# Kernel tuning notes

Hardware: AMD Instinct MI355X
Metric: run time of the kernel (lower is better)

The kernel has to match this reference:

```python
import jax, jax.numpy as jnp
import numpy as np


def setup_inputs() -> dict:
    key = jax.random.key(0)
    k1, k2 = jax.random.split(key)
    x = jax.random.normal(k1, (4096, 1024), dtype=jnp.float32)  # [B, D] queries
    y = jax.random.normal(k2, (8192, 1024), dtype=jnp.float32)  # [N, D] database
    return {"x": x, "y": y}


def reference(x, y):
    # -sum((x[:, None, :] - y[None, :, :])**2, -1)  computed via the
    x_sq = jnp.sum(x * x, axis=-1)              # [B]
    y_sq = jnp.sum(y * y, axis=-1)              # [N]
    xy = jnp.einsum('bd,nd->bn', x, y)          # [B, N]
    return -(x_sq[:, None] - 2.0 * xy + y_sq[None, :])  # [B, N]
```

## Files before the change

### kernel.cpp

```cpp
#include <hip/hip_runtime.h>
#include <hip/hip_bf16.h>


typedef __attribute__((ext_vector_type(4))) int i32x4;

#define BM 256
#define BN 256
#define KD 1024
#define NT 8

__device__ __forceinline__ void gld16(const void* g, void* l) {
    __builtin_amdgcn_global_load_lds(
        (const __attribute__((address_space(1))) unsigned int*)g,
        (__attribute__((address_space(3))) unsigned int*)l,
        16, 0, 0);
}

#define BAR()   asm volatile("s_barrier" ::: "memory")
#define LGKM0() asm volatile("s_waitcnt lgkmcnt(0)" ::: "memory")

__global__ __launch_bounds__(256) void prep_q(
    const float* __restrict__ x, const float* __restrict__ y,
    signed char* __restrict__ xq, signed char* __restrict__ yq,
    float* __restrict__ sx, float* __restrict__ sy,
    float* __restrict__ xsq, float* __restrict__ ysq, int M, int N)
{
    int row = blockIdx.x;
    const float* src;
    signed char* dst;
    float* nrm;
    float* scl;
    float sfac;
    if (row < M) {
        src = x + (size_t)row * KD; dst = xq + (size_t)row * KD;
        nrm = xsq + row; scl = sx + row; sfac = 2.0f;
    } else {
        int r = row - M;
        src = y + (size_t)r * KD; dst = yq + (size_t)r * KD;
        nrm = ysq + r; scl = sy + r; sfac = 1.0f;
    }
    int t = threadIdx.x;
    float4 v = ((const float4*)src)[t];
    float ss = v.x * v.x + v.y * v.y + v.z * v.z + v.w * v.w;
    float am = fmaxf(fmaxf(fabsf(v.x), fabsf(v.y)),
                     fmaxf(fabsf(v.z), fabsf(v.w)));
    #pragma unroll
    for (int off = 32; off > 0; off >>= 1) {
        ss += __shfl_down(ss, off, 64);
        am = fmaxf(am, __shfl_down(am, off, 64));
    }
    __shared__ float rs[4], rm[4];
    if ((t & 63) == 0) { rs[t >> 6] = ss; rm[t >> 6] = am; }
    __syncthreads();
    float tots = rs[0] + rs[1] + rs[2] + rs[3];
    float totm = fmaxf(fmaxf(rm[0], rm[1]), fmaxf(rm[2], rm[3]));
    float inv = totm > 0.0f ? 127.0f / totm : 0.0f;

    int q0 = (int)rintf(v.x * inv), q1 = (int)rintf(v.y * inv);
    int q2 = (int)rintf(v.z * inv), q3 = (int)rintf(v.w * inv);
    q0 = max(-127, min(127, q0)); q1 = max(-127, min(127, q1));
    q2 = max(-127, min(127, q2)); q3 = max(-127, min(127, q3));
    int packed = (q0 & 255) | ((q1 & 255) << 8) |
                 ((q2 & 255) << 16) | ((q3 & 255) << 24);
    ((int*)dst)[t] = packed;
    if (t == 0) { *nrm = tots; *scl = sfac * totm / 127.0f; }
}

__global__ __launch_bounds__(512, 2) void gemm_i8(
    const signed char* __restrict__ xq, const signed char* __restrict__ yq,
    const float* __restrict__ sx, const float* __restrict__ sy,
    const float* __restrict__ xsq, const float* __restrict__ ysq,
    float* __restrict__ out, int M, int N)
{
    __shared__ __align__(16) char lds[131072];

    const int ntm = M / BM;
    const int ntn = N / BN;
    const int bid = blockIdx.x;
    int tm, tn;
    if (ntm == 16 && ntn == 32) {
        int xcd = bid & 7, k = bid >> 3;
        tm = (xcd >> 2) * 8 + (k >> 3);
        tn = (xcd & 3) * 8 + (k & 7);
    } else {
        tm = bid / ntn;
        tn = bid % ntn;
    }

    const int tid  = threadIdx.x;
    const int wid  = tid >> 6;
    const int lane = tid & 63;
    const int wm   = wid >> 2;
    const int wn   = wid & 3;
    const int l15  = lane & 15;
    const int hi   = lane >> 4;
    const int s8   = lane & 7;

    const int r8  = lane >> 3;
    const int cbs = s8 ^ (r8 & 7);
    const signed char* aBase = xq + (size_t)(tm * BM + wid * 16 + r8) * KD + cbs * 16;
    const signed char* bBase = yq + (size_t)(tn * BN + wid * 16 + r8) * KD + cbs * 16;
    const int dstBase = wid * 2048 + lane * 16;

    #define STAGE_A(kt, h) do {                                               \
        const signed char* g_ = aBase + (size_t)(h) * 128 * KD + (size_t)(kt) * 128; \
        char* d_ = &lds[((kt) & 1) * 32768 + (h) * 16384 + dstBase];          \
        gld16(g_, d_); gld16(g_ + 8 * KD, d_ + 1024);                         \
    } while (0)
    #define STAGE_B(kt, h) do {                                               \
        const signed char* g_ = bBase + (size_t)(h) * 128 * KD + (size_t)(kt) * 128; \
        char* d_ = &lds[65536 + ((kt) & 1) * 32768 + (h) * 16384 + dstBase];  \
        gld16(g_, d_); gld16(g_ + 8 * KD, d_ + 1024);                         \
    } while (0)

    int aro[4], bro[2], xk[2];
    #pragma unroll
    for (int i = 0; i < 4; ++i) aro[i] = (wm * 64 + i * 16 + l15) * 128;
    #pragma unroll
    for (int j = 0; j < 2; ++j) bro[j] = (wn * 32 + j * 16 + l15) * 128;
    xk[0] = ((0 + hi) ^ s8) * 16;
    xk[1] = ((4 + hi) ^ s8) * 16;

    i32x4 acc[2][4][2][2] = {};
    i32x4 aF[2][4];
    i32x4 bF[2][2][2];

    #define MFMA_Q(mq, nq) do {                                              \
        _Pragma("unroll") for (int ks = 0; ks < 2; ++ks)                     \
        _Pragma("unroll") for (int i = 0; i < 4; ++i)                        \
        _Pragma("unroll") for (int j = 0; j < 2; ++j)                        \
            acc[mq][i][nq][j] = __builtin_amdgcn_mfma_i32_16x16x64_i8(       \
                aF[ks][i], bF[nq][ks][j], acc[mq][i][nq][j], 0, 0, 0);       \
    } while (0)

    STAGE_A(0, 0); STAGE_B(0, 0);
    STAGE_A(0, 1); STAGE_B(0, 1);
    STAGE_A(1, 0); STAGE_B(1, 0);
    asm volatile("s_waitcnt vmcnt(8)" ::: "memory");
    BAR();

    for (int s = 0; s < NT; ++s) {
        const int ab = (s & 1) * 32768;
        const int bb = 65536 + ab;

        #pragma unroll
        for (int ks = 0; ks < 2; ++ks) {
            #pragma unroll
            for (int i = 0; i < 4; ++i)
                aF[ks][i] = *(const i32x4*)&lds[ab + aro[i] + xk[ks]];
            #pragma unroll
            for (int j = 0; j < 2; ++j)
                bF[0][ks][j] = *(const i32x4*)&lds[bb + bro[j] + xk[ks]];
        }
        if (s + 1 < NT) STAGE_A(s + 1, 1);
        asm volatile("s_waitcnt lgkmcnt(8)" ::: "memory");
        BAR();
        LGKM0();
        __builtin_amdgcn_sched_barrier(0);
        __builtin_amdgcn_s_setprio(1);
        MFMA_Q(0, 0);
        __builtin_amdgcn_s_setprio(0);
        if (s < NT - 1) {
            asm volatile("s_waitcnt vmcnt(6)" ::: "memory");
        } else {
            asm volatile("s_waitcnt vmcnt(0)" ::: "memory");
        }
        BAR();

        #pragma unroll
        for (int ks = 0; ks < 2; ++ks)
            #pragma unroll
            for (int j = 0; j < 2; ++j)
                bF[1][ks][j] = *(const i32x4*)&lds[bb + 16384 + bro[j] + xk[ks]];
        if (s + 1 < NT) STAGE_B(s + 1, 1);
        BAR();
        LGKM0();
        __builtin_amdgcn_sched_barrier(0);
        __builtin_amdgcn_s_setprio(1);
        MFMA_Q(0, 1);
        __builtin_amdgcn_s_setprio(0);
        BAR();

        #pragma unroll
        for (int ks = 0; ks < 2; ++ks)
            #pragma unroll
            for (int i = 0; i < 4; ++i)
                aF[ks][i] = *(const i32x4*)&lds[ab + 16384 + aro[i] + xk[ks]];
        if (s + 2 < NT) STAGE_A(s + 2, 0);
        BAR();
        LGKM0();
        __builtin_amdgcn_sched_barrier(0);
        __builtin_amdgcn_s_setprio(1);
        MFMA_Q(1, 0);
        __builtin_amdgcn_s_setprio(0);
        BAR();

        if (s + 2 < NT) STAGE_B(s + 2, 0);
        __builtin_amdgcn_s_setprio(1);
        MFMA_Q(1, 1);
        __builtin_amdgcn_s_setprio(0);
        if (s < NT - 2) {
            asm volatile("s_waitcnt vmcnt(8)" ::: "memory");
        } else if (s == NT - 2) {
            asm volatile("s_waitcnt vmcnt(4)" ::: "memory");
        }
        BAR();
    }

    #pragma unroll
    for (int mq = 0; mq < 2; ++mq)
        #pragma unroll
        for (int i = 0; i < 4; ++i) {
            int r0 = tm * BM + mq * 128 + wm * 64 + i * 16 + hi * 4;
            #pragma unroll
            for (int nq = 0; nq < 2; ++nq)
                #pragma unroll
                for (int j = 0; j < 2; ++j) {
                    int c = tn * BN + nq * 128 + wn * 32 + j * 16 + l15;
                    float syv = sy[c];
                    float ysv = ysq[c];
                    #pragma unroll
                    for (int r = 0; r < 4; ++r) {
                        int row = r0 + r;
                        out[(size_t)row * N + c] =
                            sx[row] * syv * (float)acc[mq][i][nq][j][r]
                            - xsq[row] - ysv;
                    }
                }
        }
}

__global__ __launch_bounds__(256) void fallback_l2(
    const float* __restrict__ x, const float* __restrict__ y,
    float* __restrict__ out, int M, int N, int K)
{
    int tx = threadIdx.x & 15, ty = threadIdx.x >> 4;
    int row = blockIdx.y * 16 + ty;
    int col = blockIdx.x * 16 + tx;
    __shared__ float xs[16][17], ys[16][17];
    float s = 0.f;
    for (int k0 = 0; k0 < K; k0 += 16) {
        xs[ty][tx] = x[(size_t)row * K + k0 + tx];
        ys[ty][tx] = y[(size_t)(blockIdx.x * 16 + ty) * K + k0 + tx];
        __syncthreads();
        #pragma unroll
        for (int kk = 0; kk < 16; ++kk) {
            float d = xs[ty][kk] - ys[tx][kk];
            s += d * d;
        }
        __syncthreads();
    }
    out[(size_t)row * N + col] = -s;
}

extern "C" void kernel_launch(void* const* d_in, const int* in_sizes, int n_in,
                              void* d_out, int out_size, void* d_ws, size_t ws_size,
                              hipStream_t stream) {
    const float* x = (const float*)d_in[0];
    const float* y = (const float*)d_in[1];
    float* out = (float*)d_out;
    const int M = in_sizes[0] / KD;
    const int N = in_sizes[1] / KD;

    size_t need = (size_t)(M + N) * KD
                + (size_t)(M + N) * 2 * sizeof(float) + 256;
    if (ws_size >= need && M == 4096 && N == 8192) {
        char* w = (char*)d_ws;
        signed char* xq = (signed char*)w;
        signed char* yq = xq + (size_t)M * KD;
        float* sx  = (float*)(yq + (size_t)N * KD);
        float* sy  = sx + M;
        float* xsq = sy + N;
        float* ysq = xsq + M;

        prep_q<<<M + N, 256, 0, stream>>>(x, y, xq, yq, sx, sy, xsq, ysq, M, N);
        int grid = (M / BM) * (N / BN);
        gemm_i8<<<grid, 512, 0, stream>>>(xq, yq, sx, sy, xsq, ysq, out, M, N);
    } else {
        dim3 g(N / 16, M / 16);
        fallback_l2<<<g, 256, 0, stream>>>(x, y, out, M, N, KD);
    }
}
```

Baseline: 66.43 us.

## Replace hand-scheduled 8-wave i8 GEMM with simple 16-wave double-buffered loop

The int8 GEMM moves from 512 threads (8 waves, each owning a 2x2 set of quadrant sub-tiles) to 1024 threads (16 waves in a 4x4 grid, each owning a 64x64 output sub-tile). The hand-interleaved quadrant pipeline with explicit vmcnt/lgkmcnt waits and raw s_barriers is replaced by a plain double-buffered loop that prefetches the next K-tile, then runs 32 MFMAs per step and ends each step with __syncthreads. The goal is simpler code and more waves to hide latency in place of manual scheduling. The cost is fewer accumulator registers per wave under the new launch bounds and less fine-grained overlap of loads with MFMAs. The new launch bounds (1024, 4) request more resident waves than the 128 KiB LDS tile per block likely allows, so that occupancy may not be reached.

```diff
diff --git a/kernel.cpp b/kernel.cpp
--- a/kernel.cpp
+++ b/kernel.cpp
@@ -15,9 +15,6 @@
         (__attribute__((address_space(3))) unsigned int*)l,
         16, 0, 0);
 }
-
-#define BAR()   asm volatile("s_barrier" ::: "memory")
-#define LGKM0() asm volatile("s_waitcnt lgkmcnt(0)" ::: "memory")
 
 __global__ __launch_bounds__(256) void prep_q(
     const float* __restrict__ x, const float* __restrict__ y,
@@ -66,7 +63,7 @@
     if (t == 0) { *nrm = tots; *scl = sfac * totm / 127.0f; }
 }
 
-__global__ __launch_bounds__(512, 2) void gemm_i8(
+__global__ __launch_bounds__(1024, 4) void gemm_i8(
     const signed char* __restrict__ xq, const signed char* __restrict__ yq,
     const float* __restrict__ sx, const float* __restrict__ sy,
     const float* __restrict__ xsq, const float* __restrict__ ysq,
@@ -90,144 +87,82 @@
     const int tid  = threadIdx.x;
     const int wid  = tid >> 6;
     const int lane = tid & 63;
-    const int wm   = wid >> 2;
-    const int wn   = wid & 3;
+    const int wr   = wid >> 2;
+    const int wc   = wid & 3;
     const int l15  = lane & 15;
     const int hi   = lane >> 4;
-    const int s8   = lane & 7;
-
-    const int r8  = lane >> 3;
-    const int cbs = s8 ^ (r8 & 7);
-    const signed char* aBase = xq + (size_t)(tm * BM + wid * 16 + r8) * KD + cbs * 16;
-    const signed char* bBase = yq + (size_t)(tn * BN + wid * 16 + r8) * KD + cbs * 16;
-    const int dstBase = wid * 2048 + lane * 16;
-
-    #define STAGE_A(kt, h) do {                                               \
-        const signed char* g_ = aBase + (size_t)(h) * 128 * KD + (size_t)(kt) * 128; \
-        char* d_ = &lds[((kt) & 1) * 32768 + (h) * 16384 + dstBase];          \
-        gld16(g_, d_); gld16(g_ + 8 * KD, d_ + 1024);                         \
+
+    const int r128 = tid >> 3;
+    const int cbs  = (tid & 7) ^ (r128 & 7);
+    const signed char* aBase = xq + (size_t)(tm * BM + r128) * KD + cbs * 16;
+    const signed char* bBase = yq + (size_t)(tn * BN + r128) * KD + cbs * 16;
+    const int dstB = tid * 16;
+
+    #define STAGE(kt, buf) do {                                               \
+        const signed char* ga_ = aBase + (size_t)(kt) * 128;                  \
+        const signed char* gb_ = bBase + (size_t)(kt) * 128;                  \
+        char* da_ = &lds[(buf) * 32768 + dstB];                               \
+        char* db_ = &lds[65536 + (buf) * 32768 + dstB];                       \
+        gld16(ga_, da_); gld16(ga_ + 128 * KD, da_ + 16384);                  \
+        gld16(gb_, db_); gld16(gb_ + 128 * KD, db_ + 16384);                  \
     } while (0)
-    #define STAGE_B(kt, h) do {                                               \
-        const signed char* g_ = bBase + (size_t)(h) * 128 * KD + (size_t)(kt) * 128; \
-        char* d_ = &lds[65536 + ((kt) & 1) * 32768 + (h) * 16384 + dstBase];  \
-        gld16(g_, d_); gld16(g_ + 8 * KD, d_ + 1024);                         \
-    } while (0)
-
-    int aro[4], bro[2], xk[2];
-    #pragma unroll
-    for (int i = 0; i < 4; ++i) aro[i] = (wm * 64 + i * 16 + l15) * 128;
-    #pragma unroll
-    for (int j = 0; j < 2; ++j) bro[j] = (wn * 32 + j * 16 + l15) * 128;
-    xk[0] = ((0 + hi) ^ s8) * 16;
-    xk[1] = ((4 + hi) ^ s8) * 16;
-
-    i32x4 acc[2][4][2][2] = {};
-    i32x4 aF[2][4];
-    i32x4 bF[2][2][2];
-
-    #define MFMA_Q(mq, nq) do {                                              \
-        _Pragma("unroll") for (int ks = 0; ks < 2; ++ks)                     \
-        _Pragma("unroll") for (int i = 0; i < 4; ++i)                        \
-        _Pragma("unroll") for (int j = 0; j < 2; ++j)                        \
-            acc[mq][i][nq][j] = __builtin_amdgcn_mfma_i32_16x16x64_i8(       \
-                aF[ks][i], bF[nq][ks][j], acc[mq][i][nq][j], 0, 0, 0);       \
-    } while (0)
-
-    STAGE_A(0, 0); STAGE_B(0, 0);
-    STAGE_A(0, 1); STAGE_B(0, 1);
-    STAGE_A(1, 0); STAGE_B(1, 0);
-    asm volatile("s_waitcnt vmcnt(8)" ::: "memory");
-    BAR();
-
-    for (int s = 0; s < NT; ++s) {
-        const int ab = (s & 1) * 32768;
-        const int bb = 65536 + ab;
+
+    int aro[4], bro[4], xk[2];
+    #pragma unroll
+    for (int mi = 0; mi < 4; ++mi) aro[mi] = (wr * 64 + mi * 16 + l15) * 128;
+    #pragma unroll
+    for (int nj = 0; nj < 4; ++nj) bro[nj] = (wc * 64 + nj * 16 + l15) * 128;
+    xk[0] = ((0 + hi) ^ (l15 & 7)) * 16;
+    xk[1] = ((4 + hi) ^ (l15 & 7)) * 16;
+
+    i32x4 acc[4][4] = {};
+
+    STAGE(0, 0);
+    __syncthreads();
+
+    int buf = 0;
+    for (int t = 0; t < NT; ++t) {
+        if (t + 1 < NT) STAGE(t + 1, buf ^ 1);
+        const int ab = buf * 32768;
 
         #pragma unroll
         for (int ks = 0; ks < 2; ++ks) {
-            #pragma unroll
-            for (int i = 0; i < 4; ++i)
-                aF[ks][i] = *(const i32x4*)&lds[ab + aro[i] + xk[ks]];
-            #pragma unroll
-            for (int j = 0; j < 2; ++j)
-                bF[0][ks][j] = *(const i32x4*)&lds[bb + bro[j] + xk[ks]];
+            i32x4 aF[4], bF[4];
+            #pragma unroll
+            for (int mi = 0; mi < 4; ++mi)
+                aF[mi] = *(const i32x4*)&lds[ab + aro[mi] + xk[ks]];
+            #pragma unroll
+            for (int nj = 0; nj < 4; ++nj)
+                bF[nj] = *(const i32x4*)&lds[65536 + ab + bro[nj] + xk[ks]];
+            __builtin_amdgcn_s_setprio(1);
+            #pragma unroll
+            for (int mi = 0; mi < 4; ++mi)
+                #pragma unroll
+                for (int nj = 0; nj < 4; ++nj)
+                    acc[mi][nj] = __builtin_amdgcn_mfma_i32_16x16x64_i8(
+                        aF[mi], bF[nj], acc[mi][nj], 0, 0, 0);
+            __builtin_amdgcn_s_setprio(0);
         }
-        if (s + 1 < NT) STAGE_A(s + 1, 1);
-        asm volatile("s_waitcnt lgkmcnt(8)" ::: "memory");
-        BAR();
-        LGKM0();
-        __builtin_amdgcn_sched_barrier(0);
-        __builtin_amdgcn_s_setprio(1);
-        MFMA_Q(0, 0);
-        __builtin_amdgcn_s_setprio(0);
-        if (s < NT - 1) {
-            asm volatile("s_waitcnt vmcnt(6)" ::: "memory");
-        } else {
-            asm volatile("s_waitcnt vmcnt(0)" ::: "memory");
+        __syncthreads();
+        buf ^= 1;
+    }
+
+    #pragma unroll
+    for (int mi = 0; mi < 4; ++mi) {
+        int r0 = tm * BM + wr * 64 + mi * 16 + hi * 4;
+        #pragma unroll
+        for (int nj = 0; nj < 4; ++nj) {
+            int c = tn * BN + wc * 64 + nj * 16 + l15;
+            float syv = sy[c];
+            float ysv = ysq[c];
+            #pragma unroll
+            for (int r = 0; r < 4; ++r) {
+                int row = r0 + r;
+                out[(size_t)row * N + c] =
+                    sx[row] * syv * (float)acc[mi][nj][r] - xsq[row] - ysv;
+            }
         }
-        BAR();
-
-        #pragma unroll
-        for (int ks = 0; ks < 2; ++ks)
-            #pragma unroll
-            for (int j = 0; j < 2; ++j)
-                bF[1][ks][j] = *(const i32x4*)&lds[bb + 16384 + bro[j] + xk[ks]];
-        if (s + 1 < NT) STAGE_B(s + 1, 1);
-        BAR();
-        LGKM0();
-        __builtin_amdgcn_sched_barrier(0);
-        __builtin_amdgcn_s_setprio(1);
-        MFMA_Q(0, 1);
-        __builtin_amdgcn_s_setprio(0);
-        BAR();
-
-        #pragma unroll
-        for (int ks = 0; ks < 2; ++ks)
-            #pragma unroll
-            for (int i = 0; i < 4; ++i)
-                aF[ks][i] = *(const i32x4*)&lds[ab + 16384 + aro[i] + xk[ks]];
-        if (s + 2 < NT) STAGE_A(s + 2, 0);
-        BAR();
-        LGKM0();
-        __builtin_amdgcn_sched_barrier(0);
-        __builtin_amdgcn_s_setprio(1);
-        MFMA_Q(1, 0);
-        __builtin_amdgcn_s_setprio(0);
-        BAR();
-
-        if (s + 2 < NT) STAGE_B(s + 2, 0);
-        __builtin_amdgcn_s_setprio(1);
-        MFMA_Q(1, 1);
-        __builtin_amdgcn_s_setprio(0);
-        if (s < NT - 2) {
-            asm volatile("s_waitcnt vmcnt(8)" ::: "memory");
-        } else if (s == NT - 2) {
-            asm volatile("s_waitcnt vmcnt(4)" ::: "memory");
-        }
-        BAR();
-    }
-
-    #pragma unroll
-    for (int mq = 0; mq < 2; ++mq)
-        #pragma unroll
-        for (int i = 0; i < 4; ++i) {
-            int r0 = tm * BM + mq * 128 + wm * 64 + i * 16 + hi * 4;
-            #pragma unroll
-            for (int nq = 0; nq < 2; ++nq)
-                #pragma unroll
-                for (int j = 0; j < 2; ++j) {
-                    int c = tn * BN + nq * 128 + wn * 32 + j * 16 + l15;
-                    float syv = sy[c];
-                    float ysv = ysq[c];
-                    #pragma unroll
-                    for (int r = 0; r < 4; ++r) {
-                        int row = r0 + r;
-                        out[(size_t)row * N + c] =
-                            sx[row] * syv * (float)acc[mq][i][nq][j][r]
-                            - xsq[row] - ysv;
-                    }
-                }
-        }
+    }
 }
 
 __global__ __launch_bounds__(256) void fallback_l2(
@@ -275,7 +210,7 @@
 
         prep_q<<<M + N, 256, 0, stream>>>(x, y, xq, yq, sx, sy, xsq, ysq, M, N);
         int grid = (M / BM) * (N / BN);
-        gemm_i8<<<grid, 512, 0, stream>>>(xq, yq, sx, sy, xsq, ysq, out, M, N);
+        gemm_i8<<<grid, 1024, 0, stream>>>(xq, yq, sx, sy, xsq, ysq, out, M, N);
     } else {
         dim3 g(N / 16, M / 16);
         fallback_l2<<<g, 256, 0, stream>>>(x, y, out, M, N, KD);
```

Result: no change. 67.25 us (+1.2%).

## Restructure int8 GEMM main loop into register double-buffered k-substep pipeline

Applied to the files above, without the earlier changes.

Replaces the four-quadrant schedule, which had many barriers and explicit lgkmcnt waits, with a loop that stages a whole K tile at once. It double-buffers fragment registers across the two k-substeps so LDS reads for the next substep overlap the MFMAs of the current one. The loop is fully unrolled and has one vmcnt(0) wait plus one barrier per iteration. It doubles fragment register usage and waits on all global loads each tile, which may expose more memory latency.

```diff
diff --git a/kernel.cpp b/kernel.cpp
--- a/kernel.cpp
+++ b/kernel.cpp
@@ -16,8 +16,7 @@
         16, 0, 0);
 }
 
-#define BAR()   asm volatile("s_barrier" ::: "memory")
-#define LGKM0() asm volatile("s_waitcnt lgkmcnt(0)" ::: "memory")
+#define BAR() asm volatile("s_barrier" ::: "memory")
 
 __global__ __launch_bounds__(256) void prep_q(
     const float* __restrict__ x, const float* __restrict__ y,
@@ -122,89 +121,54 @@
     xk[1] = ((4 + hi) ^ s8) * 16;
 
     i32x4 acc[2][4][2][2] = {};
-    i32x4 aF[2][4];
-    i32x4 bF[2][2][2];
-
-    #define MFMA_Q(mq, nq) do {                                              \
-        _Pragma("unroll") for (int ks = 0; ks < 2; ++ks)                     \
+    i32x4 fA0[8], fB0[4];
+    i32x4 fA1[8], fB1[4];
+
+    #define READS(FA, FB, AB, BB, KS) do {                                   \
+        _Pragma("unroll") for (int h = 0; h < 2; ++h)                        \
         _Pragma("unroll") for (int i = 0; i < 4; ++i)                        \
+            FA[h * 4 + i] = *(const i32x4*)&lds[(AB) + h * 16384 + aro[i] + xk[KS]]; \
+        _Pragma("unroll") for (int h = 0; h < 2; ++h)                        \
+        _Pragma("unroll") for (int j = 0; j < 2; ++j)                        \
+            FB[h * 2 + j] = *(const i32x4*)&lds[(BB) + h * 16384 + bro[j] + xk[KS]]; \
+    } while (0)
+
+    #define MFMA_SET(FA, FB) do {                                            \
+        __builtin_amdgcn_s_setprio(1);                                       \
+        _Pragma("unroll") for (int mq = 0; mq < 2; ++mq)                     \
+        _Pragma("unroll") for (int i = 0; i < 4; ++i)                        \
+        _Pragma("unroll") for (int nq = 0; nq < 2; ++nq)                     \
         _Pragma("unroll") for (int j = 0; j < 2; ++j)                        \
             acc[mq][i][nq][j] = __builtin_amdgcn_mfma_i32_16x16x64_i8(       \
-                aF[ks][i], bF[nq][ks][j], acc[mq][i][nq][j], 0, 0, 0);       \
-    } while (0)
-
-    STAGE_A(0, 0); STAGE_B(0, 0);
-    STAGE_A(0, 1); STAGE_B(0, 1);
-    STAGE_A(1, 0); STAGE_B(1, 0);
-    asm volatile("s_waitcnt vmcnt(8)" ::: "memory");
+                FA[mq * 4 + i], FB[nq * 2 + j], acc[mq][i][nq][j], 0, 0, 0); \
+        __builtin_amdgcn_s_setprio(0);                                       \
+    } while (0)
+
+    STAGE_A(0, 0); STAGE_A(0, 1); STAGE_B(0, 0); STAGE_B(0, 1);
+    asm volatile("s_waitcnt vmcnt(0)" ::: "memory");
     BAR();
-
-    for (int s = 0; s < NT; ++s) {
-        const int ab = (s & 1) * 32768;
-        const int bb = 65536 + ab;
-
-        #pragma unroll
-        for (int ks = 0; ks < 2; ++ks) {
-            #pragma unroll
-            for (int i = 0; i < 4; ++i)
-                aF[ks][i] = *(const i32x4*)&lds[ab + aro[i] + xk[ks]];
-            #pragma unroll
-            for (int j = 0; j < 2; ++j)
-                bF[0][ks][j] = *(const i32x4*)&lds[bb + bro[j] + xk[ks]];
-        }
-        if (s + 1 < NT) STAGE_A(s + 1, 1);
-        asm volatile("s_waitcnt lgkmcnt(8)" ::: "memory");
-        BAR();
-        LGKM0();
-        __builtin_amdgcn_sched_barrier(0);
-        __builtin_amdgcn_s_setprio(1);
-        MFMA_Q(0, 0);
-        __builtin_amdgcn_s_setprio(0);
-        if (s < NT - 1) {
-            asm volatile("s_waitcnt vmcnt(6)" ::: "memory");
-        } else {
+    READS(fA0, fB0, 0, 65536, 0);
+
+    #pragma unroll
+    for (int k = 0; k < NT; ++k) {
+        const int ab  = (k & 1) * 32768;
+        const int bb  = 65536 + ab;
+        const int abn = ((k + 1) & 1) * 32768;
+        const int bbn = 65536 + abn;
+
+        if (k + 1 < NT) {
+            STAGE_A(k + 1, 0); STAGE_A(k + 1, 1);
+            STAGE_B(k + 1, 0); STAGE_B(k + 1, 1);
+        }
+        READS(fA1, fB1, ab, bb, 1);
+        MFMA_SET(fA0, fB0);
+
+        if (k + 1 < NT) {
             asm volatile("s_waitcnt vmcnt(0)" ::: "memory");
-        }
-        BAR();
-
-        #pragma unroll
-        for (int ks = 0; ks < 2; ++ks)
-            #pragma unroll
-            for (int j = 0; j < 2; ++j)
-                bF[1][ks][j] = *(const i32x4*)&lds[bb + 16384 + bro[j] + xk[ks]];
-        if (s + 1 < NT) STAGE_B(s + 1, 1);
-        BAR();
-        LGKM0();
-        __builtin_amdgcn_sched_barrier(0);
-        __builtin_amdgcn_s_setprio(1);
-        MFMA_Q(0, 1);
-        __builtin_amdgcn_s_setprio(0);
-        BAR();
-
-        #pragma unroll
-        for (int ks = 0; ks < 2; ++ks)
-            #pragma unroll
-            for (int i = 0; i < 4; ++i)
-                aF[ks][i] = *(const i32x4*)&lds[ab + 16384 + aro[i] + xk[ks]];
-        if (s + 2 < NT) STAGE_A(s + 2, 0);
-        BAR();
-        LGKM0();
-        __builtin_amdgcn_sched_barrier(0);
-        __builtin_amdgcn_s_setprio(1);
-        MFMA_Q(1, 0);
-        __builtin_amdgcn_s_setprio(0);
-        BAR();
-
-        if (s + 2 < NT) STAGE_B(s + 2, 0);
-        __builtin_amdgcn_s_setprio(1);
-        MFMA_Q(1, 1);
-        __builtin_amdgcn_s_setprio(0);
-        if (s < NT - 2) {
-            asm volatile("s_waitcnt vmcnt(8)" ::: "memory");
-        } else if (s == NT - 2) {
-            asm volatile("s_waitcnt vmcnt(4)" ::: "memory");
-        }
-        BAR();
+            BAR();
+            READS(fA0, fB0, abn, bbn, 0);
+        }
+        MFMA_SET(fA1, fB1);
     }
 
     #pragma unroll
```

After: 64.14 us, median of 2. 3.4% less time.
